# Kernel tuning notes

Measured on AMD Instinct MI355X. Metric: run time of the kernel, lower is better.

## Reference

```python
import jax, jax.numpy as jnp
import numpy as np

B, S, D, DH = 4, 2048, 1024, 64


def setup_inputs() -> dict:
    key = jax.random.key(0)
    ks = jax.random.split(key, 7)
    x = jax.random.normal(ks[0], (B, S, D), dtype=jnp.float32)
    def w(k):
        return jax.random.normal(k, (D, DH), dtype=jnp.float32) / np.sqrt(D).astype(np.float32)
    return {
        'x': x,
        'w_q_u': w(ks[1]), 'w_k_u': w(ks[2]), 'w_v_u': w(ks[3]),
        'w_q_c': w(ks[4]), 'w_k_c': w(ks[5]), 'w_v_c': w(ks[6]),
    }


def reference(x, w_q_u, w_k_u, w_v_u, w_q_c, w_k_c, w_v_c):
    b, n, _ = x.shape
    scale = w_q_u.shape[-1] ** -0.5
    # projections (LinearNoBias -> plain matmul)
    Q_u = x @ w_q_u
    K_u = x @ w_k_u
    V_u = x @ w_v_u
    Q_c = x @ w_q_c
    K_c = x @ w_k_c
    V_c = x @ w_v_c

    i = jnp.arange(n)
    causal = i[:, None] >= i[None, :]        # True where j <= i (binary causal / keep for S_c)
    lookahead = i[:, None] < i[None, :]      # True where j > i (allowed in sigmoid term)

    # term1: [b, n, n], zeroed above the diagonal via binary causal mask
    term1 = jnp.einsum('bid,bjd->bij', Q_c, V_u) * scale * causal.astype(x.dtype)

    # sigmoid gate: lookahead mask adds -inf on/below the diagonal -> sigmoid = 0 there
    logits_u = jnp.einsum('bid,bjd->bij', Q_u, K_u) * scale
    sigmoid_term = jax.nn.sigmoid(jnp.where(lookahead, logits_u, -jnp.inf))

    # nested n^3 matmul: S_u[b,i,k] = sum_j term1[b,i,j] * sigmoid_term[b,k,j]
    S_u = jnp.einsum('bij,bkj->bik', term1, sigmoid_term)

    S_c = jnp.where(causal, jnp.einsum('bid,bjd->bij', Q_c, K_c) * scale, -jnp.inf)

    attn = jax.nn.softmax(S_c - jax.nn.silu(S_u), axis=-1)
    return jnp.einsum('bij,bjd->bid', attn, V_c)
```

## Files before the change

kernel.cpp:

```cpp
#include <hip/hip_runtime.h>
#include <hip/hip_bf16.h>

typedef short bf16x8 __attribute__((ext_vector_type(8)));
typedef float f32x4  __attribute__((ext_vector_type(4)));
typedef _Float16 f16x8 __attribute__((ext_vector_type(8)));

#define MFMA16(a,b,c)  __builtin_amdgcn_mfma_f32_16x16x32_bf16((a),(b),(c),0,0,0)
#define MFMAF16(a,b,c) __builtin_amdgcn_mfma_f32_16x16x32_f16((a),(b),(c),0,0,0)

#define GLDS16(g,l) __builtin_amdgcn_global_load_lds( \
    (const __attribute__((address_space(1))) void*)(g), \
    (__attribute__((address_space(3))) void*)(l), 16, 0, 0)

__device__ __forceinline__ short f2bf(float f){
  union { float f; unsigned u; } v; v.f = f;
  unsigned r = v.u + 0x7fffu + ((v.u >> 16) & 1u);
  return (short)(r >> 16);
}
__device__ __forceinline__ float bf2f(short h){
  union { unsigned u; float f; } v; v.u = ((unsigned)(unsigned short)h) << 16;
  return v.f;
}
__device__ __forceinline__ void split8v(f32x4 a, f32x4 b, bf16x8& h, bf16x8& l){
  float t[8] = {a[0],a[1],a[2],a[3],b[0],b[1],b[2],b[3]};
  #pragma unroll
  for (int e = 0; e < 8; ++e){
    short hs = f2bf(t[e]);
    h[e] = hs;
    l[e] = f2bf(t[e] - bf2f(hs));
  }
}

__global__ void k_prep(const float* w0, const float* w1, const float* w2,
                       const float* w3, const float* w4, const float* w5,
                       const float* __restrict__ x,
                       unsigned short* __restrict__ wth, unsigned short* __restrict__ wtl,
                       unsigned short* __restrict__ xh, unsigned short* __restrict__ xl){
  int gb = blockIdx.x;
  if (gb < 1536){
    int p = gb >> 8;
    const float* wp = p==0?w0:p==1?w1:p==2?w2:p==3?w3:p==4?w4:w5;
    int idx = (gb & 255)*256 + threadIdx.x;
    int n = idx >> 10, k = idx & 1023;
    float v = wp[k*64 + n];
    short hs = f2bf(v);
    wth[(size_t)p*65536 + n*1024 + k] = (unsigned short)hs;
    wtl[(size_t)p*65536 + n*1024 + k] = (unsigned short)f2bf(v - bf2f(hs));
  } else {
    size_t i = ((size_t)(gb - 1536)*256 + threadIdx.x)*8;
    f32x4 a = *(const f32x4*)(x + i);
    f32x4 b = *(const f32x4*)(x + i + 4);
    bf16x8 h, l;
    split8v(a, b, h, l);
    *(bf16x8*)(xh + i) = h;
    *(bf16x8*)(xl + i) = l;
  }
}

__global__ __launch_bounds__(256) void k_proj(
    const unsigned short* __restrict__ xh, const unsigned short* __restrict__ xl,
    const unsigned short* __restrict__ wth, const unsigned short* __restrict__ wtl,
    unsigned short* __restrict__ projh, unsigned short* __restrict__ projl,
    _Float16* __restrict__ vct, _Float16* __restrict__ vuth, _Float16* __restrict__ vutl){
  __shared__ __align__(16) char sm[49152];
  int blk = blockIdx.x;
  int rb = blk/3, pg = blk - rb*3;
  int tid = threadIdx.x, w = tid >> 6, lane = tid & 63;
  int lm = lane & 15, quad = lane >> 4;
  int srow = lane >> 3, scg = (lane & 7) ^ srow;
  const char* xhg = (const char*)xh;
  const char* xlg = (const char*)xl;
  const char* w0h = (const char*)wth + (size_t)(pg*2  )*131072;
  const char* w0l = (const char*)wtl + (size_t)(pg*2  )*131072;
  const char* w1h = (const char*)wth + (size_t)(pg*2+1)*131072;
  const char* w1l = (const char*)wtl + (size_t)(pg*2+1)*131072;
  f32x4 acc[2][4] = {};
  for (int k0 = 0; k0 < 1024; k0 += 64){
    __syncthreads();
    size_t cb = (size_t)k0*2 + scg*16;
    #pragma unroll
    for (int i2 = 0; i2 < 2; ++i2){
      int i = w*2 + i2;
      size_t gx = (size_t)(rb*64 + i*8 + srow)*2048 + cb;
      size_t gw = (size_t)(i*8 + srow)*2048 + cb;
      GLDS16(xhg + gx, sm +         i*1024);
      GLDS16(xlg + gx, sm +  8192 + i*1024);
      GLDS16(w0h + gw, sm + 16384 + i*1024);
      GLDS16(w0l + gw, sm + 24576 + i*1024);
      GLDS16(w1h + gw, sm + 32768 + i*1024);
      GLDS16(w1l + gw, sm + 40960 + i*1024);
    }
    __syncthreads();
    #pragma unroll
    for (int ks = 0; ks < 2; ++ks){
      int ra = w*16 + lm;
      int offa = ra*128 + (((ks*4+quad) ^ (ra&7))*16);
      bf16x8 ah = *(const bf16x8*)(sm + offa);
      bf16x8 al = *(const bf16x8*)(sm + 8192 + offa);
      #pragma unroll
      for (int sub = 0; sub < 2; ++sub){
        #pragma unroll
        for (int n = 0; n < 4; ++n){
          int r = n*16 + lm;
          int off = r*128 + (((ks*4+quad) ^ (r&7))*16);
          bf16x8 bh = *(const bf16x8*)(sm + 16384 + sub*16384 + off);
          bf16x8 bl = *(const bf16x8*)(sm + 24576 + sub*16384 + off);
          acc[sub][n] = MFMA16(ah, bh, acc[sub][n]);
          acc[sub][n] = MFMA16(ah, bl, acc[sub][n]);
          acc[sub][n] = MFMA16(al, bh, acc[sub][n]);
        }
      }
    }
  }
  #pragma unroll
  for (int sub = 0; sub < 2; ++sub){
    int p = pg*2 + sub;
    if (p != 5){
      unsigned short* oph = projh + (size_t)p*524288;
      unsigned short* opl = projl + (size_t)p*524288;
      #pragma unroll
      for (int n = 0; n < 4; ++n)
        #pragma unroll
        for (int e = 0; e < 4; ++e){
          int r = rb*64 + w*16 + quad*4 + e;
          float f = acc[sub][n][e];
          short hs = f2bf(f);
          oph[(size_t)r*64 + n*16 + lm] = (unsigned short)hs;
          opl[(size_t)r*64 + n*16 + lm] = (unsigned short)f2bf(f - bf2f(hs));
        }
    }
  }
  if (pg == 1 || pg == 2){
    int sub = (pg == 1) ? 0 : 1;
    float (*T)[65] = (float (*)[65])sm;
    __syncthreads();
    #pragma unroll
    for (int n = 0; n < 4; ++n)
      #pragma unroll
      for (int e = 0; e < 4; ++e)
        T[w*16 + quad*4 + e][n*16 + lm] = acc[sub][n][e];
    __syncthreads();
    int b2 = rb >> 5, sl = (rb & 31)*64;
    int d = tid >> 2, sp = (tid & 3)*16;
    size_t o = (size_t)b2*131072 + (size_t)d*2048 + sl + sp;
    if (sub == 1){
      f16x8 h0, h1;
      #pragma unroll
      for (int j = 0; j < 8; ++j) h0[j] = (_Float16)T[sp + j][d];
      #pragma unroll
      for (int j = 0; j < 8; ++j) h1[j] = (_Float16)T[sp + 8 + j][d];
      *(f16x8*)(vct + o) = h0; *(f16x8*)(vct + o + 8) = h1;
    } else {
      f16x8 h0, h1, l0, l1;
      #pragma unroll
      for (int j = 0; j < 8; ++j){
        float f = T[sp + j][d];
        _Float16 h = (_Float16)f;
        h0[j] = h; l0[j] = (_Float16)(f - (float)h);
      }
      #pragma unroll
      for (int j = 0; j < 8; ++j){
        float f = T[sp + 8 + j][d];
        _Float16 h = (_Float16)f;
        h1[j] = h; l1[j] = (_Float16)(f - (float)h);
      }
      *(f16x8*)(vuth + o) = h0; *(f16x8*)(vuth + o + 8) = h1;
      *(f16x8*)(vutl + o) = l0; *(f16x8*)(vutl + o + 8) = l1;
    }
  }
}

__global__ __launch_bounds__(256,2) void k_p2(
    const unsigned short* __restrict__ ph, const unsigned short* __restrict__ pl,
    const _Float16* __restrict__ vuth, const _Float16* __restrict__ vutl,
    _Float16* __restrict__ sg, _Float16* __restrict__ t1d, float* __restrict__ W){
  __shared__ __align__(16) char sm[65536];
  int b = blockIdx.y;
  int t = blockIdx.x;
  bool isSig = t < 136;
  int a = 0, bb = 0;
  if (isSig){
    #pragma unroll 1
    for (int aa = 0; aa < 16; ++aa){
      int c = 16 - aa;
      if (t < c){ a = aa; bb = aa + t; break; }
      t -= c;
    }
  } else {
    a = bb = t - 136;
  }
  int pa = isSig ? 0 : 3;
  int pb = isSig ? 1 : 2;
  const char* Ahg = (const char*)ph + (size_t)pa*1048576;
  const char* Alg = (const char*)pl + (size_t)pa*1048576;
  const char* Bhg = (const char*)ph + (size_t)pb*1048576;
  const char* Blg = (const char*)pl + (size_t)pb*1048576;
  int tid = threadIdx.x, w = tid >> 6, lane = tid & 63;
  int lm = lane & 15, quad = lane >> 4;
  int srow = lane >> 3, scg = (lane & 7) ^ srow;
  int wm = (w & 1)*64, wn = (w >> 1)*64;
  #pragma unroll
  for (int i2 = 0; i2 < 4; ++i2){
    int i = w*4 + i2;
    int rl = i*8 + srow;
    size_t ga = (size_t)(b*2048 + a*128  + rl)*128 + scg*16;
    size_t gb = (size_t)(b*2048 + bb*128 + rl)*128 + scg*16;
    GLDS16(Ahg + ga, sm +         i*1024);
    GLDS16(Alg + ga, sm + 16384 + i*1024);
    GLDS16(Bhg + gb, sm + 32768 + i*1024);
    GLDS16(Blg + gb, sm + 49152 + i*1024);
  }
  __syncthreads();
  f32x4 acc[4][4] = {};
  #pragma unroll
  for (int ks = 0; ks < 2; ++ks){
    bf16x8 bh[4], bl[4];
    #pragma unroll
    for (int n = 0; n < 4; ++n){
      int r = wn + n*16 + lm;
      int off = r*128 + (((ks*4+quad) ^ (r&7))*16);
      bh[n] = *(const bf16x8*)(sm + 32768 + off);
      bl[n] = *(const bf16x8*)(sm + 49152 + off);
    }
    #pragma unroll
    for (int m = 0; m < 4; ++m){
      int r = wm + m*16 + lm;
      int off = r*128 + (((ks*4+quad) ^ (r&7))*16);
      bf16x8 ah = *(const bf16x8*)(sm + off);
      bf16x8 al = *(const bf16x8*)(sm + 16384 + off);
      #pragma unroll
      for (int n = 0; n < 4; ++n){
        acc[m][n] = MFMA16(ah, bh[n], acc[m][n]);
        acc[m][n] = MFMA16(ah, bl[n], acc[m][n]);
        acc[m][n] = MFMA16(al, bh[n], acc[m][n]);
      }
    }
  }
  __syncthreads();
  #pragma unroll
  for (int m = 0; m < 4; ++m){
    #pragma unroll
    for (int n = 0; n < 4; ++n){
      #pragma unroll
      for (int e = 0; e < 4; ++e){
        int il = wm + m*16 + quad*4 + e;
        int jl = wn + n*16 + lm;
        int gi = a*128 + il, gj = bb*128 + jl;
        float v = acc[m][n][e];
        float outv;
        if (isSig) outv = (gj >  gi) ? (1.0f/(1.0f + __expf(-v*0.125f))) : 0.0f;
        else       outv = (gj <= gi) ? v : 0.0f;
        *(_Float16*)(sm + ((il*256 + jl*2) ^ ((il & 7) << 4))) = (_Float16)outv;
      }
    }
  }
  __syncthreads();
  char* outp = isSig
    ? (char*)(sg + (size_t)b*4194304 + (size_t)(a*128)*2048 + bb*128)
    : (char*)t1d + (size_t)(b*16 + a)*32768;
  size_t rstride = isSig ? 4096 : 256;
  #pragma unroll
  for (int r = 0; r < 8; ++r){
    int lrow = w*32 + r*4 + (lane >> 4);
    int c16 = lane & 15;
    f32x4 vv = *(const f32x4*)(sm + ((lrow*256 + c16*16) ^ ((lrow & 7) << 4)));
    *(f32x4*)(outp + (size_t)lrow*rstride + c16*16) = vv;
  }
  if (isSig){
    int wm2 = (w & 1)*64, wn2 = (w >> 1)*32;
    f32x4 acc2[4][2] = {};
    #pragma unroll
    for (int ks = 0; ks < 4; ++ks){
      f16x8 bh2[2], bl2[2];
      #pragma unroll
      for (int n = 0; n < 2; ++n){
        int d = wn2 + n*16 + lm;
        size_t jo = ((size_t)(b*64 + d)*2048 + bb*128 + ks*32 + quad*8)*2;
        bh2[n] = *(const f16x8*)((const char*)vuth + jo);
        bl2[n] = *(const f16x8*)((const char*)vutl + jo);
      }
      #pragma unroll
      for (int m = 0; m < 4; ++m){
        int k = wm2 + m*16 + lm;
        f16x8 af = *(const f16x8*)(sm + ((k*256 + ks*64 + quad*16) ^ ((k & 7) << 4)));
        #pragma unroll
        for (int n = 0; n < 2; ++n){
          acc2[m][n] = MFMAF16(af, bh2[n], acc2[m][n]);
          acc2[m][n] = MFMAF16(af, bl2[n], acc2[m][n]);
        }
      }
    }
    float* Wp = W + (size_t)(b*136 + bb*(bb+1)/2 + a)*8192;
    #pragma unroll
    for (int m = 0; m < 4; ++m)
      #pragma unroll
      for (int n = 0; n < 2; ++n)
        #pragma unroll
        for (int e = 0; e < 4; ++e){
          int r = wm2 + m*16 + quad*4 + e;
          int col = wn2 + n*16 + lm;
          Wp[r*64 + col] = acc2[m][n][e];
        }
  }
}

__global__ __launch_bounds__(256) void k_scan(const float* __restrict__ W,
    unsigned short* __restrict__ Ph, unsigned short* __restrict__ Pl){
  int g = blockIdx.x, b = blockIdx.y;
  int ck = g >> 2, ksub = g & 3;
  if (ck >= 15) return;
  int tid = threadIdx.x;
  int rl = ksub*32 + (tid >> 3);
  int col = (tid & 7)*8;
  float acc[8] = {};
  #pragma unroll 1
  for (int c = ck; c < 15; ++c){
    const float* wt = W + (size_t)(b*136 + c*(c+1)/2 + ck)*8192 + rl*64 + col;
    f32x4 v0 = *(const f32x4*)wt;
    f32x4 v1 = *(const f32x4*)(wt + 4);
    #pragma unroll
    for (int e = 0; e < 4; ++e){ acc[e] += v0[e]; acc[4+e] += v1[e]; }
    size_t o = ((size_t)(b*16 + c + 1)*2048 + ck*128 + rl)*64 + col;
    bf16x8 h, l;
    #pragma unroll
    for (int e = 0; e < 8; ++e){
      short hs = f2bf(acc[e]);
      h[e] = hs;
      l[e] = f2bf(acc[e] - bf2f(hs));
    }
    *(bf16x8*)(Ph + o) = h;
    *(bf16x8*)(Pl + o) = l;
  }
}

__global__ __launch_bounds__(256,2) void k_p3(
    const unsigned short* __restrict__ ph, const unsigned short* __restrict__ pl,
    const _Float16* __restrict__ t1d, const _Float16* __restrict__ sg,
    const unsigned short* __restrict__ Ph, const unsigned short* __restrict__ Pl,
    _Float16* __restrict__ lg){
  __shared__ __align__(16) char sm[32768];
  int t = blockIdx.x, b = blockIdx.y;
  int ci = 0, ck = 0;
  #pragma unroll 1
  for (int aa = 0; aa < 16; ++aa){
    if (t < aa + 1){ ci = aa; ck = t; break; }
    t -= aa + 1;
  }
  int tid = threadIdx.x, w = tid >> 6, lane = tid & 63;
  int lm = lane & 15, quad = lane >> 4;
  int wm = (w & 1)*64, wn = (w >> 1)*64;
  f32x4 su[4][4] = {}, sc[4][4] = {};

  const char* Qh = (const char*)ph + (size_t)3*1048576;
  const char* Ql = (const char*)pl + (size_t)3*1048576;
  const char* Kh = (const char*)ph + (size_t)4*1048576;
  const char* Kl = (const char*)pl + (size_t)4*1048576;

  #pragma unroll
  for (int ks = 0; ks < 2; ++ks){
    bf16x8 kh[4], kl[4];
    #pragma unroll
    for (int n = 0; n < 4; ++n){
      size_t off = (size_t)(b*2048 + ck*128 + wn + n*16 + lm)*128 + (ks*32 + quad*8)*2;
      kh[n] = *(const bf16x8*)(Kh + off);
      kl[n] = *(const bf16x8*)(Kl + off);
    }
    #pragma unroll
    for (int m = 0; m < 4; ++m){
      size_t off = (size_t)(b*2048 + ci*128 + wm + m*16 + lm)*128 + (ks*32 + quad*8)*2;
      bf16x8 ah = *(const bf16x8*)(Qh + off);
      bf16x8 al = *(const bf16x8*)(Ql + off);
      #pragma unroll
      for (int n = 0; n < 4; ++n){
        sc[m][n] = MFMA16(ah, kh[n], sc[m][n]);
        sc[m][n] = MFMA16(ah, kl[n], sc[m][n]);
        sc[m][n] = MFMA16(al, kh[n], sc[m][n]);
      }
    }
  }
  if (ck < ci){
    #pragma unroll
    for (int ks = 0; ks < 2; ++ks){
      bf16x8 bh[4], bl[4];
      #pragma unroll
      for (int n = 0; n < 4; ++n){
        size_t off = (((size_t)(b*16 + ci)*2048 + ck*128 + wn + n*16 + lm)*64 + ks*32 + quad*8)*2;
        bh[n] = *(const bf16x8*)((const char*)Ph + off);
        bl[n] = *(const bf16x8*)((const char*)Pl + off);
      }
      #pragma unroll
      for (int m = 0; m < 4; ++m){
        size_t off = (size_t)(b*2048 + ci*128 + wm + m*16 + lm)*128 + (ks*32 + quad*8)*2;
        bf16x8 ah = *(const bf16x8*)(Qh + off);
        bf16x8 al = *(const bf16x8*)(Ql + off);
        #pragma unroll
        for (int n = 0; n < 4; ++n){
          su[m][n] = MFMA16(ah, bh[n], su[m][n]);
          su[m][n] = MFMA16(ah, bl[n], su[m][n]);
          su[m][n] = MFMA16(al, bh[n], su[m][n]);
        }
      }
    }
  }
  const char* t1b = (const char*)t1d + (size_t)(b*16 + ci)*32768;
  const char* sgb = (const char*)sg + (size_t)b*8388608;
  #pragma unroll
  for (int ks = 0; ks < 4; ++ks){
    f16x8 bs[4];
    #pragma unroll
    for (int n = 0; n < 4; ++n)
      bs[n] = *(const f16x8*)(sgb + ((size_t)(ck*128 + wn + n*16 + lm)*2048 + ci*128 + ks*32 + quad*8)*2);
    #pragma unroll
    for (int m = 0; m < 4; ++m){
      f16x8 at = *(const f16x8*)(t1b + ((wm + m*16 + lm)*128 + ks*32 + quad*8)*2);
      #pragma unroll
      for (int n = 0; n < 4; ++n)
        su[m][n] = MFMAF16(at, bs[n], su[m][n]);
    }
  }
  _Float16* Tt = (_Float16*)sm;
  #pragma unroll
  for (int m = 0; m < 4; ++m)
    #pragma unroll
    for (int n = 0; n < 4; ++n)
      #pragma unroll
      for (int e = 0; e < 4; ++e){
        int il = wm + m*16 + quad*4 + e;
        int jl = wn + n*16 + lm;
        float xv = 0.125f*su[m][n][e];
        float sg1 = 1.0f/(1.0f + __expf(-xv));
        Tt[il*128 + jl] = (_Float16)(sc[m][n][e]*0.125f - xv*sg1);
      }
  __syncthreads();
  _Float16* lgb = lg + (size_t)b*4194304;
  #pragma unroll
  for (int r = 0; r < 8; ++r){
    int lrow = w*32 + r*4 + (lane >> 4);
    int c16 = lane & 15;
    f32x4 vv = *(const f32x4*)(sm + lrow*256 + c16*16);
    *(f32x4*)((char*)(lgb + (size_t)(ci*128 + lrow)*2048 + ck*128) + c16*16) = vv;
  }
}

__global__ __launch_bounds__(256,2) void k_p4(const _Float16* __restrict__ lg,
    const _Float16* __restrict__ vct, float* __restrict__ out){
  __shared__ __align__(16) char sm[66048];
  float* Mz = (float*)(sm + 65536);
  float* Sz = (float*)(sm + 65792);
  int b = blockIdx.y;
  int b1 = blockIdx.x;
  int tid = threadIdx.x, w = tid >> 6, lane = tid & 63;
  int lm = lane & 15, quad = lane >> 4;
  const _Float16* vb = vct + (size_t)b*131072;
  for (int pass = 0; pass < 2; ++pass){
    int band = pass ? (127 - b1) : b1;
    int r0 = band*16;
    const char* lgb = (const char*)lg + ((size_t)b*4194304 + (size_t)r0*2048)*2;
    int nkt = ((r0 + 15) >> 6) + 1;
    int fc = (r0 + 1) >> 6;
    int srl = lane >> 3, ssl = lane & 7;
    __syncthreads();
    for (int kt = w; kt < nkt; kt += 4){
      #pragma unroll
      for (int i2 = 0; i2 < 2; ++i2){
        int rl = i2*8 + srl;
        GLDS16(lgb + (size_t)rl*4096 + kt*128 + ((ssl ^ (rl & 7))*16),
               sm + kt*2048 + i2*1024);
      }
    }
    __syncthreads();
    float m_r = -3.0e38f;
    for (int kt = w; kt < nkt; kt += 4){
      #pragma unroll
      for (int half = 0; half < 2; ++half){
        int sl = quad*2 + half;
        f16x8 v = *(const f16x8*)(sm + kt*2048 + lm*128 + ((sl ^ (lm & 7))*16));
        int cb = kt*64 + sl*8;
        #pragma unroll
        for (int e = 0; e < 8; ++e)
          m_r = (cb + e <= r0 + lm) ? fmaxf(m_r, (float)v[e]) : m_r;
      }
    }
    m_r = fmaxf(m_r, __shfl_xor(m_r, 16));
    m_r = fmaxf(m_r, __shfl_xor(m_r, 32));
    Mz[w*16 + lm] = m_r;
    __syncthreads();
    float mfin = fmaxf(fmaxf(Mz[lm], Mz[16 + lm]), fmaxf(Mz[32 + lm], Mz[48 + lm]));
    float s_r = 0.0f;
    for (int kt = w; kt < nkt; kt += 4){
      #pragma unroll
      for (int half = 0; half < 2; ++half){
        int sl = quad*2 + half;
        f16x8 v = *(const f16x8*)(sm + kt*2048 + lm*128 + ((sl ^ (lm & 7))*16));
        int cb = kt*64 + sl*8;
        #pragma unroll
        for (int e = 0; e < 8; ++e)
          if (cb + e <= r0 + lm) s_r += __expf((float)v[e] - mfin);
      }
    }
    s_r += __shfl_xor(s_r, 16);
    s_r += __shfl_xor(s_r, 32);
    Sz[w*16 + lm] = s_r;
    f32x4 acc[4] = {};
    for (int kt = w; kt < nkt; kt += 4){
      bool full = kt < fc;
      #pragma unroll
      for (int ks = 0; ks < 2; ++ks){
        f16x8 Lv = *(const f16x8*)(sm + kt*2048 + lm*128 + (((ks*4+quad) ^ (lm & 7))*16));
        int jbase = kt*64 + ks*32 + quad*8;
        f16x8 af;
        #pragma unroll
        for (int e = 0; e < 8; ++e){
          float p = __expf((float)Lv[e] - mfin);
          if (!full && (jbase + e > r0 + lm)) p = 0.0f;
          af[e] = (_Float16)p;
        }
        #pragma unroll
        for (int n = 0; n < 4; ++n){
          f16x8 bv = *(const f16x8*)(vb + (size_t)(n*16 + lm)*2048 + jbase);
          acc[n] = MFMAF16(af, bv, acc[n]);
        }
      }
    }
    __syncthreads();
    float* Ot = (float*)sm;
    #pragma unroll
    for (int n = 0; n < 4; ++n)
      #pragma unroll
      for (int e = 0; e < 4; ++e)
        Ot[(w*16 + quad*4 + e)*64 + n*16 + lm] = acc[n][e];
    __syncthreads();
    int row = tid >> 4, c4 = (tid & 15)*4;
    f32x4 s = *(const f32x4*)&Ot[row*64 + c4];
    #pragma unroll
    for (int ww = 1; ww < 4; ++ww){
      f32x4 t2 = *(const f32x4*)&Ot[(ww*16 + row)*64 + c4];
      s[0]+=t2[0]; s[1]+=t2[1]; s[2]+=t2[2]; s[3]+=t2[3];
    }
    float z = Sz[row] + Sz[16 + row] + Sz[32 + row] + Sz[48 + row];
    f32x4 o = { s[0]/z, s[1]/z, s[2]/z, s[3]/z };
    *(f32x4*)(out + ((size_t)b*2048 + r0 + row)*64 + c4) = o;
  }
}

static const size_t OFF_WTH   = 4194304;
static const size_t OFF_WTL   = 4980736;
static const size_t OFF_PROJH = 5767168;
static const size_t OFF_PROJL = 12058624;
static const size_t OFF_VCT   = 18350080;
static const size_t OFF_SG    = 19398656;
static const size_t OFF_LG    = 52953088;
static const size_t OFF_T1D   = 86507520;
static const size_t OFF_PH    = 88604672;
static const size_t OFF_PL    = 105381888;
static const size_t OFF_VUTH  = 122159104;
static const size_t OFF_VUTL  = 123207680;
static const size_t OFF_XH    = 124256256;
static const size_t OFF_XL    = 141033472;
static const size_t OFF_W     = OFF_XH;

extern "C" void kernel_launch(void* const* d_in, const int* in_sizes, int n_in,
                              void* d_out, int out_size, void* d_ws, size_t ws_size,
                              hipStream_t stream){
  (void)in_sizes; (void)n_in; (void)out_size; (void)ws_size;
  const float* x = (const float*)d_in[0];
  char* ws = (char*)d_ws;
  unsigned short* wth   = (unsigned short*)(ws + OFF_WTH);
  unsigned short* wtl   = (unsigned short*)(ws + OFF_WTL);
  unsigned short* projh = (unsigned short*)(ws + OFF_PROJH);
  unsigned short* projl = (unsigned short*)(ws + OFF_PROJL);
  _Float16*       vct   = (_Float16*)(ws + OFF_VCT);
  _Float16*       sg    = (_Float16*)(ws + OFF_SG);
  _Float16*       lg    = (_Float16*)(ws + OFF_LG);
  _Float16*       t1d   = (_Float16*)(ws + OFF_T1D);
  unsigned short* Phb   = (unsigned short*)(ws + OFF_PH);
  unsigned short* Plb   = (unsigned short*)(ws + OFF_PL);
  _Float16*       vuth  = (_Float16*)(ws + OFF_VUTH);
  _Float16*       vutl  = (_Float16*)(ws + OFF_VUTL);
  unsigned short* xh    = (unsigned short*)(ws + OFF_XH);
  unsigned short* xl    = (unsigned short*)(ws + OFF_XL);
  float*          Wb    = (float*)(ws + OFF_W);

  k_prep  <<<dim3(5632),   256, 0, stream>>>((const float*)d_in[1], (const float*)d_in[2],
                                             (const float*)d_in[3], (const float*)d_in[4],
                                             (const float*)d_in[5], (const float*)d_in[6],
                                             x, wth, wtl, xh, xl);
  k_proj  <<<dim3(384),    256, 0, stream>>>(xh, xl, wth, wtl, projh, projl, vct, vuth, vutl);
  k_p2    <<<dim3(152,4),  256, 0, stream>>>(projh, projl, vuth, vutl, sg, t1d, Wb);
  k_scan  <<<dim3(64,4),   256, 0, stream>>>(Wb, Phb, Plb);
  k_p3    <<<dim3(136,4),  256, 0, stream>>>(projh, projl, t1d, sg, Phb, Plb, lg);
  k_p4    <<<dim3(64,4),   256, 0, stream>>>(lg, vct, (float*)d_out);
}
```

Baseline: 205.8 us.

## Drop LDS staging in k_p2 and split k_p3 tiles into row halves

k_p2 no longer stages its A/B operand tiles through LDS with global_load_lds. It reads the bf16 fragments straight from global memory, which halves shared memory and raises the launch bound to 3 blocks per CU. k_p3 now splits each 128x128 output tile into two 64-row halves, giving twice as many blocks, half the accumulators per thread, 16KB of LDS and a launch bound of 4 blocks per CU. The aim is more occupancy and better load balance. The cost is redundant, uncoalesced global operand reads where the LDS reuse used to be, and K/P operands that both halves of a k_p3 tile now reload.

```diff
diff --git a/kernel.cpp b/kernel.cpp
--- a/kernel.cpp
+++ b/kernel.cpp
@@ -170,11 +170,11 @@
   }
 }
 
-__global__ __launch_bounds__(256,2) void k_p2(
+__global__ __launch_bounds__(256,3) void k_p2(
     const unsigned short* __restrict__ ph, const unsigned short* __restrict__ pl,
     const _Float16* __restrict__ vuth, const _Float16* __restrict__ vutl,
     _Float16* __restrict__ sg, _Float16* __restrict__ t1d, float* __restrict__ W){
-  __shared__ __align__(16) char sm[65536];
+  __shared__ __align__(16) char sm[32768];
   int b = blockIdx.y;
   int t = blockIdx.x;
   bool isSig = t < 136;
@@ -197,37 +197,22 @@
   const char* Blg = (const char*)pl + (size_t)pb*1048576;
   int tid = threadIdx.x, w = tid >> 6, lane = tid & 63;
   int lm = lane & 15, quad = lane >> 4;
-  int srow = lane >> 3, scg = (lane & 7) ^ srow;
   int wm = (w & 1)*64, wn = (w >> 1)*64;
-  #pragma unroll
-  for (int i2 = 0; i2 < 4; ++i2){
-    int i = w*4 + i2;
-    int rl = i*8 + srow;
-    size_t ga = (size_t)(b*2048 + a*128  + rl)*128 + scg*16;
-    size_t gb = (size_t)(b*2048 + bb*128 + rl)*128 + scg*16;
-    GLDS16(Ahg + ga, sm +         i*1024);
-    GLDS16(Alg + ga, sm + 16384 + i*1024);
-    GLDS16(Bhg + gb, sm + 32768 + i*1024);
-    GLDS16(Blg + gb, sm + 49152 + i*1024);
-  }
-  __syncthreads();
   f32x4 acc[4][4] = {};
   #pragma unroll
   for (int ks = 0; ks < 2; ++ks){
     bf16x8 bh[4], bl[4];
     #pragma unroll
     for (int n = 0; n < 4; ++n){
-      int r = wn + n*16 + lm;
-      int off = r*128 + (((ks*4+quad) ^ (r&7))*16);
-      bh[n] = *(const bf16x8*)(sm + 32768 + off);
-      bl[n] = *(const bf16x8*)(sm + 49152 + off);
+      size_t off = (size_t)(b*2048 + bb*128 + wn + n*16 + lm)*128 + (ks*32 + quad*8)*2;
+      bh[n] = *(const bf16x8*)(Bhg + off);
+      bl[n] = *(const bf16x8*)(Blg + off);
     }
     #pragma unroll
     for (int m = 0; m < 4; ++m){
-      int r = wm + m*16 + lm;
-      int off = r*128 + (((ks*4+quad) ^ (r&7))*16);
-      bf16x8 ah = *(const bf16x8*)(sm + off);
-      bf16x8 al = *(const bf16x8*)(sm + 16384 + off);
+      size_t off = (size_t)(b*2048 + a*128 + wm + m*16 + lm)*128 + (ks*32 + quad*8)*2;
+      bf16x8 ah = *(const bf16x8*)(Ahg + off);
+      bf16x8 al = *(const bf16x8*)(Alg + off);
       #pragma unroll
       for (int n = 0; n < 4; ++n){
         acc[m][n] = MFMA16(ah, bh[n], acc[m][n]);
@@ -236,7 +221,6 @@
       }
     }
   }
-  __syncthreads();
   #pragma unroll
   for (int m = 0; m < 4; ++m){
     #pragma unroll
@@ -333,23 +317,25 @@
   }
 }
 
-__global__ __launch_bounds__(256,2) void k_p3(
+__global__ __launch_bounds__(256,4) void k_p3(
     const unsigned short* __restrict__ ph, const unsigned short* __restrict__ pl,
     const _Float16* __restrict__ t1d, const _Float16* __restrict__ sg,
     const unsigned short* __restrict__ Ph, const unsigned short* __restrict__ Pl,
     _Float16* __restrict__ lg){
-  __shared__ __align__(16) char sm[32768];
+  __shared__ __align__(16) char sm[16384];
   int t = blockIdx.x, b = blockIdx.y;
+  int pr = t >> 1, hh = t & 1;
   int ci = 0, ck = 0;
   #pragma unroll 1
   for (int aa = 0; aa < 16; ++aa){
-    if (t < aa + 1){ ci = aa; ck = t; break; }
-    t -= aa + 1;
+    if (pr < aa + 1){ ci = aa; ck = pr; break; }
+    pr -= aa + 1;
   }
   int tid = threadIdx.x, w = tid >> 6, lane = tid & 63;
   int lm = lane & 15, quad = lane >> 4;
-  int wm = (w & 1)*64, wn = (w >> 1)*64;
-  f32x4 su[4][4] = {}, sc[4][4] = {};
+  int wn = w*32;
+  int rbase = ci*128 + hh*64;
+  f32x4 su[4][2] = {}, sc[4][2] = {};
 
   const char* Qh = (const char*)ph + (size_t)3*1048576;
   const char* Ql = (const char*)pl + (size_t)3*1048576;
@@ -358,20 +344,20 @@
 
   #pragma unroll
   for (int ks = 0; ks < 2; ++ks){
-    bf16x8 kh[4], kl[4];
-    #pragma unroll
-    for (int n = 0; n < 4; ++n){
+    bf16x8 kh[2], kl[2];
+    #pragma unroll
+    for (int n = 0; n < 2; ++n){
       size_t off = (size_t)(b*2048 + ck*128 + wn + n*16 + lm)*128 + (ks*32 + quad*8)*2;
       kh[n] = *(const bf16x8*)(Kh + off);
       kl[n] = *(const bf16x8*)(Kl + off);
     }
     #pragma unroll
     for (int m = 0; m < 4; ++m){
-      size_t off = (size_t)(b*2048 + ci*128 + wm + m*16 + lm)*128 + (ks*32 + quad*8)*2;
+      size_t off = (size_t)(b*2048 + rbase + m*16 + lm)*128 + (ks*32 + quad*8)*2;
       bf16x8 ah = *(const bf16x8*)(Qh + off);
       bf16x8 al = *(const bf16x8*)(Ql + off);
       #pragma unroll
-      for (int n = 0; n < 4; ++n){
+      for (int n = 0; n < 2; ++n){
         sc[m][n] = MFMA16(ah, kh[n], sc[m][n]);
         sc[m][n] = MFMA16(ah, kl[n], sc[m][n]);
         sc[m][n] = MFMA16(al, kh[n], sc[m][n]);
@@ -381,20 +367,20 @@
   if (ck < ci){
     #pragma unroll
     for (int ks = 0; ks < 2; ++ks){
-      bf16x8 bh[4], bl[4];
-      #pragma unroll
-      for (int n = 0; n < 4; ++n){
+      bf16x8 bh[2], bl[2];
+      #pragma unroll
+      for (int n = 0; n < 2; ++n){
         size_t off = (((size_t)(b*16 + ci)*2048 + ck*128 + wn + n*16 + lm)*64 + ks*32 + quad*8)*2;
         bh[n] = *(const bf16x8*)((const char*)Ph + off);
         bl[n] = *(const bf16x8*)((const char*)Pl + off);
       }
       #pragma unroll
       for (int m = 0; m < 4; ++m){
-        size_t off = (size_t)(b*2048 + ci*128 + wm + m*16 + lm)*128 + (ks*32 + quad*8)*2;
+        size_t off = (size_t)(b*2048 + rbase + m*16 + lm)*128 + (ks*32 + quad*8)*2;
         bf16x8 ah = *(const bf16x8*)(Qh + off);
         bf16x8 al = *(const bf16x8*)(Ql + off);
         #pragma unroll
-        for (int n = 0; n < 4; ++n){
+        for (int n = 0; n < 2; ++n){
           su[m][n] = MFMA16(ah, bh[n], su[m][n]);
           su[m][n] = MFMA16(ah, bl[n], su[m][n]);
           su[m][n] = MFMA16(al, bh[n], su[m][n]);
@@ -406,15 +392,15 @@
   const char* sgb = (const char*)sg + (size_t)b*8388608;
   #pragma unroll
   for (int ks = 0; ks < 4; ++ks){
-    f16x8 bs[4];
-    #pragma unroll
-    for (int n = 0; n < 4; ++n)
+    f16x8 bs[2];
+    #pragma unroll
+    for (int n = 0; n < 2; ++n)
       bs[n] = *(const f16x8*)(sgb + ((size_t)(ck*128 + wn + n*16 + lm)*2048 + ci*128 + ks*32 + quad*8)*2);
     #pragma unroll
     for (int m = 0; m < 4; ++m){
-      f16x8 at = *(const f16x8*)(t1b + ((wm + m*16 + lm)*128 + ks*32 + quad*8)*2);
-      #pragma unroll
-      for (int n = 0; n < 4; ++n)
+      f16x8 at = *(const f16x8*)(t1b + ((hh*64 + m*16 + lm)*128 + ks*32 + quad*8)*2);
+      #pragma unroll
+      for (int n = 0; n < 2; ++n)
         su[m][n] = MFMAF16(at, bs[n], su[m][n]);
     }
   }
@@ -422,10 +408,10 @@
   #pragma unroll
   for (int m = 0; m < 4; ++m)
     #pragma unroll
-    for (int n = 0; n < 4; ++n)
+    for (int n = 0; n < 2; ++n)
       #pragma unroll
       for (int e = 0; e < 4; ++e){
-        int il = wm + m*16 + quad*4 + e;
+        int il = m*16 + quad*4 + e;
         int jl = wn + n*16 + lm;
         float xv = 0.125f*su[m][n][e];
         float sg1 = 1.0f/(1.0f + __expf(-xv));
@@ -434,11 +420,11 @@
   __syncthreads();
   _Float16* lgb = lg + (size_t)b*4194304;
   #pragma unroll
-  for (int r = 0; r < 8; ++r){
-    int lrow = w*32 + r*4 + (lane >> 4);
+  for (int r = 0; r < 4; ++r){
+    int lrow = w*16 + r*4 + (lane >> 4);
     int c16 = lane & 15;
     f32x4 vv = *(const f32x4*)(sm + lrow*256 + c16*16);
-    *(f32x4*)((char*)(lgb + (size_t)(ci*128 + lrow)*2048 + ck*128) + c16*16) = vv;
+    *(f32x4*)((char*)(lgb + (size_t)(rbase + lrow)*2048 + ck*128) + c16*16) = vv;
   }
 }
 
@@ -588,6 +574,6 @@
   k_proj  <<<dim3(384),    256, 0, stream>>>(xh, xl, wth, wtl, projh, projl, vct, vuth, vutl);
   k_p2    <<<dim3(152,4),  256, 0, stream>>>(projh, projl, vuth, vutl, sg, t1d, Wb);
   k_scan  <<<dim3(64,4),   256, 0, stream>>>(Wb, Phb, Plb);
-  k_p3    <<<dim3(136,4),  256, 0, stream>>>(projh, projl, t1d, sg, Phb, Plb, lg);
+  k_p3    <<<dim3(272,4),  256, 0, stream>>>(projh, projl, t1d, sg, Phb, Plb, lg);
   k_p4    <<<dim3(64,4),   256, 0, stream>>>(lg, vct, (float*)d_out);
 }
```

Result: slower. 212.7 us (+3.3%).

## Load p2 operands directly from global, remap p3 tile order, fuse Q loads

Applied to the files above, without the earlier changes.

In k_p2 the global-to-LDS staging of the A and B projection tiles is removed. Operands are now read straight from global memory into registers, which halves shared memory so the kernel can target three blocks per CU instead of two. In k_p3 the block index is permuted so that neighbouring blocks take different causal tiles, and the S_c and S_u products are merged into one loop that reuses the loaded Q fragments. The trade-off is more direct global and L2 traffic in k_p2, plus higher register pressure in k_p3 from holding the K and P fragments at the same time.

```diff
diff --git a/kernel.cpp b/kernel.cpp
--- a/kernel.cpp
+++ b/kernel.cpp
@@ -170,11 +170,11 @@
   }
 }
 
-__global__ __launch_bounds__(256,2) void k_p2(
+__global__ __launch_bounds__(256,3) void k_p2(
     const unsigned short* __restrict__ ph, const unsigned short* __restrict__ pl,
     const _Float16* __restrict__ vuth, const _Float16* __restrict__ vutl,
     _Float16* __restrict__ sg, _Float16* __restrict__ t1d, float* __restrict__ W){
-  __shared__ __align__(16) char sm[65536];
+  __shared__ __align__(16) char sm[32768];
   int b = blockIdx.y;
   int t = blockIdx.x;
   bool isSig = t < 136;
@@ -197,37 +197,22 @@
   const char* Blg = (const char*)pl + (size_t)pb*1048576;
   int tid = threadIdx.x, w = tid >> 6, lane = tid & 63;
   int lm = lane & 15, quad = lane >> 4;
-  int srow = lane >> 3, scg = (lane & 7) ^ srow;
   int wm = (w & 1)*64, wn = (w >> 1)*64;
-  #pragma unroll
-  for (int i2 = 0; i2 < 4; ++i2){
-    int i = w*4 + i2;
-    int rl = i*8 + srow;
-    size_t ga = (size_t)(b*2048 + a*128  + rl)*128 + scg*16;
-    size_t gb = (size_t)(b*2048 + bb*128 + rl)*128 + scg*16;
-    GLDS16(Ahg + ga, sm +         i*1024);
-    GLDS16(Alg + ga, sm + 16384 + i*1024);
-    GLDS16(Bhg + gb, sm + 32768 + i*1024);
-    GLDS16(Blg + gb, sm + 49152 + i*1024);
-  }
-  __syncthreads();
   f32x4 acc[4][4] = {};
   #pragma unroll
   for (int ks = 0; ks < 2; ++ks){
     bf16x8 bh[4], bl[4];
     #pragma unroll
     for (int n = 0; n < 4; ++n){
-      int r = wn + n*16 + lm;
-      int off = r*128 + (((ks*4+quad) ^ (r&7))*16);
-      bh[n] = *(const bf16x8*)(sm + 32768 + off);
-      bl[n] = *(const bf16x8*)(sm + 49152 + off);
+      size_t off = (size_t)(b*2048 + bb*128 + wn + n*16 + lm)*128 + (ks*32 + quad*8)*2;
+      bh[n] = *(const bf16x8*)(Bhg + off);
+      bl[n] = *(const bf16x8*)(Blg + off);
     }
     #pragma unroll
     for (int m = 0; m < 4; ++m){
-      int r = wm + m*16 + lm;
-      int off = r*128 + (((ks*4+quad) ^ (r&7))*16);
-      bf16x8 ah = *(const bf16x8*)(sm + off);
-      bf16x8 al = *(const bf16x8*)(sm + 16384 + off);
+      size_t off = (size_t)(b*2048 + a*128 + wm + m*16 + lm)*128 + (ks*32 + quad*8)*2;
+      bf16x8 ah = *(const bf16x8*)(Ahg + off);
+      bf16x8 al = *(const bf16x8*)(Alg + off);
       #pragma unroll
       for (int n = 0; n < 4; ++n){
         acc[m][n] = MFMA16(ah, bh[n], acc[m][n]);
@@ -236,7 +221,6 @@
       }
     }
   }
-  __syncthreads();
   #pragma unroll
   for (int m = 0; m < 4; ++m){
     #pragma unroll
@@ -339,7 +323,8 @@
     const unsigned short* __restrict__ Ph, const unsigned short* __restrict__ Pl,
     _Float16* __restrict__ lg){
   __shared__ __align__(16) char sm[32768];
-  int t = blockIdx.x, b = blockIdx.y;
+  int t0 = blockIdx.x, b = blockIdx.y;
+  int t = (t0 & 7)*17 + (t0 >> 3);
   int ci = 0, ck = 0;
   #pragma unroll 1
   for (int aa = 0; aa < 16; ++aa){
@@ -350,6 +335,7 @@
   int lm = lane & 15, quad = lane >> 4;
   int wm = (w & 1)*64, wn = (w >> 1)*64;
   f32x4 su[4][4] = {}, sc[4][4] = {};
+  bool hasP = (ck < ci);
 
   const char* Qh = (const char*)ph + (size_t)3*1048576;
   const char* Ql = (const char*)pl + (size_t)3*1048576;
@@ -358,41 +344,33 @@
 
   #pragma unroll
   for (int ks = 0; ks < 2; ++ks){
-    bf16x8 kh[4], kl[4];
+    bf16x8 kh[4], kl[4], bh[4], bl[4];
     #pragma unroll
     for (int n = 0; n < 4; ++n){
-      size_t off = (size_t)(b*2048 + ck*128 + wn + n*16 + lm)*128 + (ks*32 + quad*8)*2;
-      kh[n] = *(const bf16x8*)(Kh + off);
-      kl[n] = *(const bf16x8*)(Kl + off);
+      size_t offk = (size_t)(b*2048 + ck*128 + wn + n*16 + lm)*128 + (ks*32 + quad*8)*2;
+      kh[n] = *(const bf16x8*)(Kh + offk);
+      kl[n] = *(const bf16x8*)(Kl + offk);
+    }
+    if (hasP){
+      #pragma unroll
+      for (int n = 0; n < 4; ++n){
+        size_t offp = (((size_t)(b*16 + ci)*2048 + ck*128 + wn + n*16 + lm)*64 + ks*32 + quad*8)*2;
+        bh[n] = *(const bf16x8*)((const char*)Ph + offp);
+        bl[n] = *(const bf16x8*)((const char*)Pl + offp);
+      }
     }
     #pragma unroll
     for (int m = 0; m < 4; ++m){
-      size_t off = (size_t)(b*2048 + ci*128 + wm + m*16 + lm)*128 + (ks*32 + quad*8)*2;
-      bf16x8 ah = *(const bf16x8*)(Qh + off);
-      bf16x8 al = *(const bf16x8*)(Ql + off);
+      size_t offq = (size_t)(b*2048 + ci*128 + wm + m*16 + lm)*128 + (ks*32 + quad*8)*2;
+      bf16x8 ah = *(const bf16x8*)(Qh + offq);
+      bf16x8 al = *(const bf16x8*)(Ql + offq);
       #pragma unroll
       for (int n = 0; n < 4; ++n){
         sc[m][n] = MFMA16(ah, kh[n], sc[m][n]);
         sc[m][n] = MFMA16(ah, kl[n], sc[m][n]);
         sc[m][n] = MFMA16(al, kh[n], sc[m][n]);
       }
-    }
-  }
-  if (ck < ci){
-    #pragma unroll
-    for (int ks = 0; ks < 2; ++ks){
-      bf16x8 bh[4], bl[4];
-      #pragma unroll
-      for (int n = 0; n < 4; ++n){
-        size_t off = (((size_t)(b*16 + ci)*2048 + ck*128 + wn + n*16 + lm)*64 + ks*32 + quad*8)*2;
-        bh[n] = *(const bf16x8*)((const char*)Ph + off);
-        bl[n] = *(const bf16x8*)((const char*)Pl + off);
-      }
-      #pragma unroll
-      for (int m = 0; m < 4; ++m){
-        size_t off = (size_t)(b*2048 + ci*128 + wm + m*16 + lm)*128 + (ks*32 + quad*8)*2;
-        bf16x8 ah = *(const bf16x8*)(Qh + off);
-        bf16x8 al = *(const bf16x8*)(Ql + off);
+      if (hasP){
         #pragma unroll
         for (int n = 0; n < 4; ++n){
           su[m][n] = MFMA16(ah, bh[n], su[m][n]);
```

Measured after the change: 207.3 us. Within noise of the previous version (+0.7%).
